# Performance work log

Measured on AMD Instinct MI355X. Metric: run time of the kernel, lower is better.

Reference implementation:

```python
import jax, jax.numpy as jnp
import numpy as np

D = 128
HIDDEN = 512
N = 2048


def setup_inputs() -> dict:
    key = jax.random.key(0)
    k_x, k0, k1, k2 = jax.random.split(key, 4)
    x = jax.random.normal(k_x, (N, D), dtype=jnp.float32)
    # LocallyConnected init: uniform(-sqrt(1/in), sqrt(1/in))
    b0 = 1.0 / np.sqrt(D)
    b1 = 1.0 / np.sqrt(HIDDEN)
    W0 = jax.random.uniform(k0, (D, D, HIDDEN), jnp.float32, -b0, b0)
    W1 = jax.random.uniform(k1, (D, HIDDEN, HIDDEN), jnp.float32, -b1, b1)
    W2 = jax.random.uniform(k2, (D, HIDDEN, 1), jnp.float32, -b1, b1)
    return {"x": x, "W0": W0, "W1": W1, "W2": W2}


def reference(x, W0, W1, W2):
    n, d = x.shape
    # masking layer: matmul with diag(mask[i]) == elementwise zero-out of diagonal
    mask = 1.0 - jnp.eye(d, dtype=x.dtype)          # [d, d]
    h = x[:, None, :] * mask[None, :, :]            # [n, d, d]
    # per-node locally-connected MLP
    h = jax.nn.leaky_relu(jnp.einsum('ndi,dio->ndo', h, W0))   # [n, d, hidden]
    h = jax.nn.leaky_relu(jnp.einsum('ndi,dio->ndo', h, W1))   # [n, d, hidden]
    h = jnp.einsum('ndi,dio->ndo', h, W2)                      # [n, d, 1]
    return h.squeeze(-1)                                       # [n, d]
```

## Files before the change

### kernel.cpp

```cpp
#include <hip/hip_runtime.h>

#define DD 128
#define HH 512
#define NN 2048
#define NT 64
#define PLD 516

typedef __bf16 bf16x8 __attribute__((ext_vector_type(8)));
typedef __bf16 bf16x4 __attribute__((ext_vector_type(4)));
typedef float  floatx4  __attribute__((ext_vector_type(4)));
typedef float  floatx16 __attribute__((ext_vector_type(16)));

__global__ void cvt_x(const float* __restrict__ x, __bf16* __restrict__ xb) {
    int t = blockIdx.x * blockDim.x + threadIdx.x;
    float4 v = *(const float4*)(x + (size_t)t * 4);
    bf16x4 o;
    o[0] = (__bf16)v.x; o[1] = (__bf16)v.y; o[2] = (__bf16)v.z; o[3] = (__bf16)v.w;
    *(bf16x4*)(xb + (size_t)t * 4) = o;
}

__global__ void pack_w(const float* __restrict__ W, __bf16* __restrict__ Wp, int nks32) {
    __shared__ __bf16 Ls[32 * PLD];
    const int d  = blockIdx.x / nks32;
    const int ks = blockIdx.x % nks32;
    const int tid = threadIdx.x;
    const int nks16 = nks32 * 2;
    const float* src = W + ((size_t)(d * nks32 + ks) * 32) * HH;

#pragma unroll
    for (int it = 0; it < 16; ++it) {
        int e = (it * 256 + tid) * 4;
        float4 v = *(const float4*)(src + e);
        bf16x4 o;
        o[0] = (__bf16)v.x; o[1] = (__bf16)v.y; o[2] = (__bf16)v.z; o[3] = (__bf16)v.w;
        *(bf16x4*)(Ls + (e >> 9) * PLD + (e & 511)) = o;
    }
    __syncthreads();

#pragma unroll
    for (int it = 0; it < 8; ++it) {
        int u  = it * 256 + tid;
        int l  = u & 63;
        int ct = (u >> 6) & 15;
        int kh = u >> 10;
        int lr = l & 31, lh = l >> 5;
        bf16x8 v;
#pragma unroll
        for (int j = 0; j < 8; ++j)
            v[j] = Ls[(kh * 16 + lh * 8 + j) * PLD + ct * 32 + lr];
        *(bf16x8*)(Wp + ((size_t)(d * 16 + ct) * nks16 + (ks * 2 + kh)) * 512 + l * 8) = v;
    }
}

__launch_bounds__(512, 4)
__global__ void grandag_main(const __bf16* __restrict__ xb,
                             const __bf16* __restrict__ W0p,
                             const __bf16* __restrict__ W1p,
                             const float* __restrict__ W2,
                             float* __restrict__ out) {
    __shared__ __bf16 h1s[NT * HH];
    __shared__ float  outp2[8][NT];

    const int b  = blockIdx.x;
    const int d  = ((b >> 8) << 3) | (b & 7);
    const int n0 = ((b >> 3) & 31) * NT;

    const int tid = threadIdx.x;
    const int w   = tid >> 6;
    const int l   = tid & 63;
    const int lr  = l & 31;
    const int lh  = l >> 5;
    const int swz = lr & 7;

    const int kz  = d >> 4;
    const int lhz = (d >> 3) & 1;
    const int jz  = d & 7;

    {
        floatx16 acc[2][2] = {};
        const __bf16* W0b = W0p + ((size_t)(d * 16 + w * 2) * 8) * 512 + (size_t)l * 8;
        const __bf16* xbb = xb + (size_t)(n0 + lr) * DD + lh * 8;

        bf16x8 wa0 = *(const bf16x8*)(W0b);
        bf16x8 wa1 = *(const bf16x8*)(W0b + (size_t)8 * 512);
#pragma unroll
        for (int ks = 0; ks < 8; ks += 2) {
            bf16x8 wb0 = *(const bf16x8*)(W0b + (size_t)(ks + 1) * 512);
            bf16x8 wb1 = *(const bf16x8*)(W0b + (size_t)(8 + ks + 1) * 512);
            bf16x8 x0 = *(const bf16x8*)(xbb + (size_t)ks * 16);
            bf16x8 x1 = *(const bf16x8*)(xbb + (size_t)32 * DD + ks * 16);
            if (ks == kz && lh == lhz) {
#pragma unroll
                for (int j = 0; j < 8; j++)
                    if (j == jz) { x0[j] = (__bf16)0.f; x1[j] = (__bf16)0.f; }
            }
            acc[0][0] = __builtin_amdgcn_mfma_f32_32x32x16_bf16(wa0, x0, acc[0][0], 0, 0, 0);
            acc[0][1] = __builtin_amdgcn_mfma_f32_32x32x16_bf16(wa0, x1, acc[0][1], 0, 0, 0);
            acc[1][0] = __builtin_amdgcn_mfma_f32_32x32x16_bf16(wa1, x0, acc[1][0], 0, 0, 0);
            acc[1][1] = __builtin_amdgcn_mfma_f32_32x32x16_bf16(wa1, x1, acc[1][1], 0, 0, 0);
            wa0 = *(const bf16x8*)(W0b + (size_t)((ks + 2) & 7) * 512);
            wa1 = *(const bf16x8*)(W0b + (size_t)(8 + ((ks + 2) & 7)) * 512);
            x0 = *(const bf16x8*)(xbb + (size_t)(ks + 1) * 16);
            x1 = *(const bf16x8*)(xbb + (size_t)32 * DD + (ks + 1) * 16);
            if (ks + 1 == kz && lh == lhz) {
#pragma unroll
                for (int j = 0; j < 8; j++)
                    if (j == jz) { x0[j] = (__bf16)0.f; x1[j] = (__bf16)0.f; }
            }
            acc[0][0] = __builtin_amdgcn_mfma_f32_32x32x16_bf16(wb0, x0, acc[0][0], 0, 0, 0);
            acc[0][1] = __builtin_amdgcn_mfma_f32_32x32x16_bf16(wb0, x1, acc[0][1], 0, 0, 0);
            acc[1][0] = __builtin_amdgcn_mfma_f32_32x32x16_bf16(wb1, x0, acc[1][0], 0, 0, 0);
            acc[1][1] = __builtin_amdgcn_mfma_f32_32x32x16_bf16(wb1, x1, acc[1][1], 0, 0, 0);
        }
#pragma unroll
        for (int mt = 0; mt < 2; mt++) {
#pragma unroll
            for (int q2 = 0; q2 < 4; q2++) {
                const int chunk = 8 * w + 4 * mt + q2;
#pragma unroll
                for (int nt = 0; nt < 2; nt++) {
                    const int row = nt * 32 + lr;
                    bf16x4 o;
#pragma unroll
                    for (int i = 0; i < 4; i++) {
                        float v = acc[mt][nt][q2 * 4 + i];
                        o[i] = (__bf16)fmaxf(v, 0.01f * v);
                    }
                    *(bf16x4*)(h1s + (size_t)row * HH + ((chunk ^ swz) << 3) + 4 * lh) = o;
                }
            }
        }
    }
    __syncthreads();

    floatx16 acc2[2][2] = {};
    {
        const __bf16* W1b  = W1p + ((size_t)(d * 16 + w * 2) * 32) * 512 + (size_t)l * 8;
        const __bf16* h1b0 = h1s + (size_t)lr * HH;
        const __bf16* h1b1 = h1s + (size_t)(32 + lr) * HH;

        bf16x8 wa0 = *(const bf16x8*)(W1b);
        bf16x8 wa1 = *(const bf16x8*)(W1b + (size_t)32 * 512);
#pragma unroll
        for (int ks = 0; ks < 32; ks += 2) {
            bf16x8 wb0 = *(const bf16x8*)(W1b + (size_t)(ks + 1) * 512);
            bf16x8 wb1 = *(const bf16x8*)(W1b + (size_t)(32 + ks + 1) * 512);
            bf16x8 h0  = *(const bf16x8*)(h1b0 + (((2 * ks + lh) ^ swz) << 3));
            bf16x8 h1v = *(const bf16x8*)(h1b1 + (((2 * ks + lh) ^ swz) << 3));
            acc2[0][0] = __builtin_amdgcn_mfma_f32_32x32x16_bf16(wa0, h0,  acc2[0][0], 0, 0, 0);
            acc2[0][1] = __builtin_amdgcn_mfma_f32_32x32x16_bf16(wa0, h1v, acc2[0][1], 0, 0, 0);
            acc2[1][0] = __builtin_amdgcn_mfma_f32_32x32x16_bf16(wa1, h0,  acc2[1][0], 0, 0, 0);
            acc2[1][1] = __builtin_amdgcn_mfma_f32_32x32x16_bf16(wa1, h1v, acc2[1][1], 0, 0, 0);
            wa0 = *(const bf16x8*)(W1b + (size_t)((ks + 2) & 31) * 512);
            wa1 = *(const bf16x8*)(W1b + (size_t)(32 + ((ks + 2) & 31)) * 512);
            h0  = *(const bf16x8*)(h1b0 + (((2 * (ks + 1) + lh) ^ swz) << 3));
            h1v = *(const bf16x8*)(h1b1 + (((2 * (ks + 1) + lh) ^ swz) << 3));
            acc2[0][0] = __builtin_amdgcn_mfma_f32_32x32x16_bf16(wb0, h0,  acc2[0][0], 0, 0, 0);
            acc2[0][1] = __builtin_amdgcn_mfma_f32_32x32x16_bf16(wb0, h1v, acc2[0][1], 0, 0, 0);
            acc2[1][0] = __builtin_amdgcn_mfma_f32_32x32x16_bf16(wb1, h0,  acc2[1][0], 0, 0, 0);
            acc2[1][1] = __builtin_amdgcn_mfma_f32_32x32x16_bf16(wb1, h1v, acc2[1][1], 0, 0, 0);
        }
    }

    {
        const float* W2b = W2 + (size_t)d * HH + w * 64 + lh * 4;
#pragma unroll
        for (int nt = 0; nt < 2; nt++) {
            float s = 0.f;
#pragma unroll
            for (int mt = 0; mt < 2; mt++) {
#pragma unroll
                for (int q2 = 0; q2 < 4; q2++) {
                    floatx4 w2q = *(const floatx4*)(W2b + mt * 32 + 8 * q2);
#pragma unroll
                    for (int i = 0; i < 4; i++) {
                        float v = acc2[mt][nt][q2 * 4 + i];
                        s += fmaxf(v, 0.01f * v) * w2q[i];
                    }
                }
            }
            s += __shfl_xor(s, 32, 64);
            if (!lh) outp2[w][nt * 32 + lr] = s;
        }
    }
    __syncthreads();
    if (tid < NT) {
        float v = 0.f;
#pragma unroll
        for (int ww = 0; ww < 8; ww++) v += outp2[ww][tid];
        out[(size_t)(n0 + tid) * DD + d] = v;
    }
}

extern "C" void kernel_launch(void* const* d_in, const int* in_sizes, int n_in,
                              void* d_out, int out_size, void* d_ws, size_t ws_size,
                              hipStream_t stream) {
    const float* x  = (const float*)d_in[0];
    const float* W0 = (const float*)d_in[1];
    const float* W1 = (const float*)d_in[2];
    const float* W2 = (const float*)d_in[3];
    float* out = (float*)d_out;

    __bf16* W0p = (__bf16*)d_ws;
    __bf16* W1p = (__bf16*)((char*)d_ws + (size_t)DD * DD * HH * 2);
    __bf16* xb  = (__bf16*)((char*)d_ws + (size_t)DD * DD * HH * 2
                                        + (size_t)DD * HH * HH * 2);

    cvt_x<<<dim3(NN * DD / (256 * 4)), 256, 0, stream>>>(x, xb);
    pack_w<<<dim3(DD * (DD / 32)), 256, 0, stream>>>(W0, W0p, DD / 32);
    pack_w<<<dim3(DD * (HH / 32)), 256, 0, stream>>>(W1, W1p, HH / 32);

    grandag_main<<<dim3(DD * (NN / NT)), 512, 0, stream>>>(xb, W0p, W1p, W2, out);
}
```

Before: 418.9 us.

## Stagger per-wave K start order, async-load W2 into LDS, scalarize wave id

Each wave now starts its K loop at a different offset (rotating start index) in both GEMM stages, so waves in a block read different k-slices of x/h1s at the same time. This is meant to reduce LDS bank and L2 channel contention. W2 is prefetched into shared memory with global_load_lds at kernel start, and the wave index is made wave-uniform via readfirstlane. Because the start index now differs per wave, k-offsets are runtime values rather than compile-time constants. That can add address arithmetic and shorten the prefetch distance from two steps to one. It also relies on the W2 LDS load being visible after the existing barrier.

```diff
diff --git a/kernel.cpp b/kernel.cpp
--- a/kernel.cpp
+++ b/kernel.cpp
@@ -10,6 +10,9 @@
 typedef __bf16 bf16x4 __attribute__((ext_vector_type(4)));
 typedef float  floatx4  __attribute__((ext_vector_type(4)));
 typedef float  floatx16 __attribute__((ext_vector_type(16)));
+
+typedef const __attribute__((address_space(1))) void* as1cv;
+typedef __attribute__((address_space(3))) void* as3v;
 
 __global__ void cvt_x(const float* __restrict__ x, __bf16* __restrict__ xb) {
     int t = blockIdx.x * blockDim.x + threadIdx.x;
@@ -60,13 +63,14 @@
                              float* __restrict__ out) {
     __shared__ __bf16 h1s[NT * HH];
     __shared__ float  outp2[8][NT];
+    __shared__ float  w2s[HH];
 
     const int b  = blockIdx.x;
     const int d  = ((b >> 8) << 3) | (b & 7);
     const int n0 = ((b >> 3) & 31) * NT;
 
     const int tid = threadIdx.x;
-    const int w   = tid >> 6;
+    const int wq  = __builtin_amdgcn_readfirstlane(tid >> 6);
     const int l   = tid & 63;
     const int lr  = l & 31;
     const int lh  = l >> 5;
@@ -76,20 +80,27 @@
     const int lhz = (d >> 3) & 1;
     const int jz  = d & 7;
 
+    if (wq < 2) {
+        const float* g = W2 + (size_t)d * HH + (size_t)(wq * 64 + l) * 4;
+        __builtin_amdgcn_global_load_lds((as1cv)g, (as3v)(w2s + wq * 256), 16, 0, 0);
+    }
+
     {
         floatx16 acc[2][2] = {};
-        const __bf16* W0b = W0p + ((size_t)(d * 16 + w * 2) * 8) * 512 + (size_t)l * 8;
+        const __bf16* W0b = W0p + ((size_t)(d * 16 + wq * 2) * 8) * 512 + (size_t)l * 8;
         const __bf16* xbb = xb + (size_t)(n0 + lr) * DD + lh * 8;
 
-        bf16x8 wa0 = *(const bf16x8*)(W0b);
-        bf16x8 wa1 = *(const bf16x8*)(W0b + (size_t)8 * 512);
-#pragma unroll
-        for (int ks = 0; ks < 8; ks += 2) {
-            bf16x8 wb0 = *(const bf16x8*)(W0b + (size_t)(ks + 1) * 512);
-            bf16x8 wb1 = *(const bf16x8*)(W0b + (size_t)(8 + ks + 1) * 512);
-            bf16x8 x0 = *(const bf16x8*)(xbb + (size_t)ks * 16);
-            bf16x8 x1 = *(const bf16x8*)(xbb + (size_t)32 * DD + ks * 16);
-            if (ks == kz && lh == lhz) {
+        int ke = wq & 7;
+        bf16x8 wa0 = *(const bf16x8*)(W0b + (size_t)ke * 512);
+        bf16x8 wa1 = *(const bf16x8*)(W0b + (size_t)(8 + ke) * 512);
+#pragma unroll
+        for (int i = 0; i < 8; i++) {
+            const int kn = (ke + 1) & 7;
+            bf16x8 wb0 = *(const bf16x8*)(W0b + (size_t)kn * 512);
+            bf16x8 wb1 = *(const bf16x8*)(W0b + (size_t)(8 + kn) * 512);
+            bf16x8 x0 = *(const bf16x8*)(xbb + (size_t)ke * 16);
+            bf16x8 x1 = *(const bf16x8*)(xbb + (size_t)(32 * DD) + ke * 16);
+            if (ke == kz && lh == lhz) {
 #pragma unroll
                 for (int j = 0; j < 8; j++)
                     if (j == jz) { x0[j] = (__bf16)0.f; x1[j] = (__bf16)0.f; }
@@ -98,25 +109,13 @@
             acc[0][1] = __builtin_amdgcn_mfma_f32_32x32x16_bf16(wa0, x1, acc[0][1], 0, 0, 0);
             acc[1][0] = __builtin_amdgcn_mfma_f32_32x32x16_bf16(wa1, x0, acc[1][0], 0, 0, 0);
             acc[1][1] = __builtin_amdgcn_mfma_f32_32x32x16_bf16(wa1, x1, acc[1][1], 0, 0, 0);
-            wa0 = *(const bf16x8*)(W0b + (size_t)((ks + 2) & 7) * 512);
-            wa1 = *(const bf16x8*)(W0b + (size_t)(8 + ((ks + 2) & 7)) * 512);
-            x0 = *(const bf16x8*)(xbb + (size_t)(ks + 1) * 16);
-            x1 = *(const bf16x8*)(xbb + (size_t)32 * DD + (ks + 1) * 16);
-            if (ks + 1 == kz && lh == lhz) {
-#pragma unroll
-                for (int j = 0; j < 8; j++)
-                    if (j == jz) { x0[j] = (__bf16)0.f; x1[j] = (__bf16)0.f; }
-            }
-            acc[0][0] = __builtin_amdgcn_mfma_f32_32x32x16_bf16(wb0, x0, acc[0][0], 0, 0, 0);
-            acc[0][1] = __builtin_amdgcn_mfma_f32_32x32x16_bf16(wb0, x1, acc[0][1], 0, 0, 0);
-            acc[1][0] = __builtin_amdgcn_mfma_f32_32x32x16_bf16(wb1, x0, acc[1][0], 0, 0, 0);
-            acc[1][1] = __builtin_amdgcn_mfma_f32_32x32x16_bf16(wb1, x1, acc[1][1], 0, 0, 0);
+            wa0 = wb0; wa1 = wb1; ke = kn;
         }
 #pragma unroll
         for (int mt = 0; mt < 2; mt++) {
 #pragma unroll
             for (int q2 = 0; q2 < 4; q2++) {
-                const int chunk = 8 * w + 4 * mt + q2;
+                const int chunk = 8 * wq + 4 * mt + q2;
 #pragma unroll
                 for (int nt = 0; nt < 2; nt++) {
                     const int row = nt * 32 + lr;
@@ -135,35 +134,31 @@
 
     floatx16 acc2[2][2] = {};
     {
-        const __bf16* W1b  = W1p + ((size_t)(d * 16 + w * 2) * 32) * 512 + (size_t)l * 8;
+        const __bf16* W1b  = W1p + ((size_t)(d * 16 + wq * 2) * 32) * 512 + (size_t)l * 8;
         const __bf16* h1b0 = h1s + (size_t)lr * HH;
         const __bf16* h1b1 = h1s + (size_t)(32 + lr) * HH;
 
-        bf16x8 wa0 = *(const bf16x8*)(W1b);
-        bf16x8 wa1 = *(const bf16x8*)(W1b + (size_t)32 * 512);
-#pragma unroll
-        for (int ks = 0; ks < 32; ks += 2) {
-            bf16x8 wb0 = *(const bf16x8*)(W1b + (size_t)(ks + 1) * 512);
-            bf16x8 wb1 = *(const bf16x8*)(W1b + (size_t)(32 + ks + 1) * 512);
-            bf16x8 h0  = *(const bf16x8*)(h1b0 + (((2 * ks + lh) ^ swz) << 3));
-            bf16x8 h1v = *(const bf16x8*)(h1b1 + (((2 * ks + lh) ^ swz) << 3));
+        int ke = (wq * 4) & 31;
+        bf16x8 wa0 = *(const bf16x8*)(W1b + (size_t)ke * 512);
+        bf16x8 wa1 = *(const bf16x8*)(W1b + (size_t)(32 + ke) * 512);
+#pragma unroll
+        for (int i = 0; i < 32; i++) {
+            const int kn = (ke + 1) & 31;
+            bf16x8 wb0 = *(const bf16x8*)(W1b + (size_t)kn * 512);
+            bf16x8 wb1 = *(const bf16x8*)(W1b + (size_t)(32 + kn) * 512);
+            const int hoff = ((2 * ke + lh) ^ swz) << 3;
+            bf16x8 h0  = *(const bf16x8*)(h1b0 + hoff);
+            bf16x8 h1v = *(const bf16x8*)(h1b1 + hoff);
             acc2[0][0] = __builtin_amdgcn_mfma_f32_32x32x16_bf16(wa0, h0,  acc2[0][0], 0, 0, 0);
             acc2[0][1] = __builtin_amdgcn_mfma_f32_32x32x16_bf16(wa0, h1v, acc2[0][1], 0, 0, 0);
             acc2[1][0] = __builtin_amdgcn_mfma_f32_32x32x16_bf16(wa1, h0,  acc2[1][0], 0, 0, 0);
             acc2[1][1] = __builtin_amdgcn_mfma_f32_32x32x16_bf16(wa1, h1v, acc2[1][1], 0, 0, 0);
-            wa0 = *(const bf16x8*)(W1b + (size_t)((ks + 2) & 31) * 512);
-            wa1 = *(const bf16x8*)(W1b + (size_t)(32 + ((ks + 2) & 31)) * 512);
-            h0  = *(const bf16x8*)(h1b0 + (((2 * (ks + 1) + lh) ^ swz) << 3));
-            h1v = *(const bf16x8*)(h1b1 + (((2 * (ks + 1) + lh) ^ swz) << 3));
-            acc2[0][0] = __builtin_amdgcn_mfma_f32_32x32x16_bf16(wb0, h0,  acc2[0][0], 0, 0, 0);
-            acc2[0][1] = __builtin_amdgcn_mfma_f32_32x32x16_bf16(wb0, h1v, acc2[0][1], 0, 0, 0);
-            acc2[1][0] = __builtin_amdgcn_mfma_f32_32x32x16_bf16(wb1, h0,  acc2[1][0], 0, 0, 0);
-            acc2[1][1] = __builtin_amdgcn_mfma_f32_32x32x16_bf16(wb1, h1v, acc2[1][1], 0, 0, 0);
+            wa0 = wb0; wa1 = wb1; ke = kn;
         }
     }
 
     {
-        const float* W2b = W2 + (size_t)d * HH + w * 64 + lh * 4;
+        const float* W2b = w2s + wq * 64 + lh * 4;
 #pragma unroll
         for (int nt = 0; nt < 2; nt++) {
             float s = 0.f;
@@ -180,7 +175,7 @@
                 }
             }
             s += __shfl_xor(s, 32, 64);
-            if (!lh) outp2[w][nt * 32 + lr] = s;
+            if (!lh) outp2[wq][nt * 32 + lr] = s;
         }
     }
     __syncthreads();
```

After: 418.7 us. No clear change (-0.1%).
